# Performance work log

Measured on AMD Instinct MI355X. Metric: run time of the kernel, lower is better.

## Reference

```python
import jax, jax.numpy as jnp
from jax import lax
import numpy as np

DN = ('NCHW', 'OIHW', 'NCHW')

def conv2d_same(x, w, b):
    # 5x5, stride 1, pad 2 == SAME
    y = lax.conv_general_dilated(x, w, (1, 1), 'SAME', dimension_numbers=DN)
    return y + b[None, :, None, None]

def setup_inputs() -> dict:
    key = jax.random.key(0)
    ks = jax.random.split(key, 5)
    B, S, D = 8, 2048, 1024
    k55 = 0.2  # ~1/sqrt(25) init scale
    return {
        'x':  jax.random.normal(ks[0], (B, S, D), dtype=jnp.float32),
        'w1': jax.random.normal(ks[1], (1, 1, 5, 5), dtype=jnp.float32) * k55,
        'b1': jnp.zeros((1,), jnp.float32),
        'w2': jax.random.normal(ks[2], (1, 1, 5, 5), dtype=jnp.float32) * k55,
        'b2': jnp.zeros((1,), jnp.float32),
        'w3': jax.random.normal(ks[3], (1, 2, 5, 5), dtype=jnp.float32) * k55,
        'b3': jnp.zeros((1,), jnp.float32),
        'w4': jax.random.normal(ks[4], (1, 1, 5, 5), dtype=jnp.float32) * k55,
        'b4': jnp.zeros((1,), jnp.float32),
    }

def reference(x, w1, b1, w2, b2, w3, b3, w4, b4):
    # x: [b, s, d]
    xT = jnp.swapaxes(x, 1, 2)                              # [b, d, s]
    # self-similarity, softmax over BATCH dim (dim=0, as in original)
    NSSM = jax.nn.softmax(jnp.einsum('bsd,btd->bst', x, x), axis=0)   # [b, s, s]
    conv_x  = conv2d_same(x[:, None],  w1, b1)[:, 0]        # [b, s, d]
    conv_xT = conv2d_same(xT[:, None], w2, b2)[:, 0]        # [b, d, s]
    Attention_map = jax.nn.softmax(jnp.matmul(conv_x, conv_xT), axis=0)  # [b, s, s]
    Moca_map = conv2d_same(jnp.stack([NSSM, Attention_map], axis=1), w3, b3)[:, 0]  # [b, s, s]
    conv_g = conv2d_same(x[:, None], w4, b4)[:, 0]          # [b, s, d]
    Wz = jnp.matmul(Moca_map, conv_g)                       # [b, s, d]
    return Wz + x
```

## Files before the change

### kernel.cpp

```cpp
#include <hip/hip_runtime.h>

#define Bz 8
#define Sz 2048
#define Dz 1024

typedef __attribute__((ext_vector_type(8))) _Float16 f16x8;
typedef __attribute__((ext_vector_type(8))) short short8v;
typedef __attribute__((ext_vector_type(4))) short short4v;
typedef __attribute__((ext_vector_type(4))) float f32x4;

__device__ __forceinline__ short f2h(float f) {
    _Float16 h = (_Float16)f;
    return __builtin_bit_cast(short, h);
}
__device__ __forceinline__ float h2f(short s) {
    return (float)__builtin_bit_cast(_Float16, s);
}
__device__ __forceinline__ void gld16(const void* g, void* l) {
    __builtin_amdgcn_global_load_lds(
        (const __attribute__((address_space(1))) void*)g,
        (__attribute__((address_space(3))) void*)l, 16, 0, 0);
}

__global__ __launch_bounds__(256) void conv3_kernel(
    const float* __restrict__ x,
    const float* __restrict__ w1, const float* __restrict__ b1,
    const float* __restrict__ w2, const float* __restrict__ b2,
    short* __restrict__ x16, short* __restrict__ C1f, short* __restrict__ C2f)
{
    __shared__ float w[50];
    __shared__ float bias[2];
    const size_t SD = (size_t)Sz * Dz;
    int tid = threadIdx.x;
    if (tid < 25) w[tid] = w1[tid];
    else if (tid < 50) w[tid] = w2[tid - 25];
    if (tid == 50) { bias[0] = b1[0]; bias[1] = b2[0]; }
    __syncthreads();

    int d4 = tid * 4;
    int y = blockIdx.y;
    int s = ((y & 7) << 8) | (y >> 3);
    int b = blockIdx.z;
    const float* xb = x + (size_t)b * SD + d4;

    float wv[5][12];
#pragma unroll
    for (int i = 0; i < 5; i++) {
        int ss = s + i - 2;
        int ssc = ss < 0 ? 0 : (ss >= Sz ? Sz - 1 : ss);
        const float* rp = xb + (size_t)ssc * Dz;
        if (d4 > 0) *(float4*)&wv[i][0] = *(const float4*)(rp - 4);
        else { wv[i][0] = wv[i][1] = wv[i][2] = wv[i][3] = 0.f; }
        *(float4*)&wv[i][4] = *(const float4*)rp;
        if (d4 < 1020) *(float4*)&wv[i][8] = *(const float4*)(rp + 4);
        else { wv[i][8] = wv[i][9] = wv[i][10] = wv[i][11] = 0.f; }
        if (ss != ssc) {
#pragma unroll
            for (int q = 0; q < 12; q++) wv[i][q] = 0.f;
        }
    }

    float o1[4] = {}, o2[4] = {};
#pragma unroll
    for (int i = 0; i < 5; i++)
#pragma unroll
        for (int j = 0; j < 5; j++) {
            float c1w = w[i * 5 + j], c2w = w[25 + j * 5 + i];
#pragma unroll
            for (int q = 0; q < 4; q++) {
                float v = wv[i][q + j + 2];
                o1[q] = fmaf(c1w, v, o1[q]);
                o2[q] = fmaf(c2w, v, o2[q]);
            }
        }
    size_t o = (size_t)b * SD + (size_t)s * Dz + d4;
    short4v hx, h1, h2;
#pragma unroll
    for (int q = 0; q < 4; q++) {
        hx[q] = f2h(wv[2][q + 4]);
        h1[q] = f2h(o1[q] + bias[0]);
        h2[q] = f2h(o2[q] + bias[1]);
    }
    *(short4v*)(x16 + o) = hx;
    *(short4v*)(C1f + o) = h1;
    *(short4v*)(C2f + o) = h2;
}

__global__ __launch_bounds__(256) void convT_kernel(
    const float* __restrict__ x, const float* __restrict__ w4,
    const float* __restrict__ b4, short* __restrict__ C4T)
{
    __shared__ float xs[68][73];
    __shared__ short ct[64][72];
    __shared__ float w[25];
    __shared__ float bb;
    const size_t SD = (size_t)Sz * Dz;
    int tid = threadIdx.x;
    if (tid < 25) w[tid] = w4[tid];
    if (tid == 25) bb = b4[0];

    int s0 = blockIdx.x * 64, d0 = blockIdx.y * 64, b = blockIdx.z;
    const float* xb = x + (size_t)b * SD;
    for (int k = tid; k < 68 * 68; k += 256) {
        int r = k / 68, c = k - r * 68;
        int gr = s0 - 2 + r, gc = d0 - 2 + c;
        float v = 0.f;
        if (gr >= 0 && gr < Sz && gc >= 0 && gc < Dz) v = xb[(size_t)gr * Dz + gc];
        xs[r][c] = v;
    }
    __syncthreads();

    int sl = tid & 63, dg = tid >> 6;
    float acc[16];
#pragma unroll
    for (int q = 0; q < 16; q++) acc[q] = bb;
#pragma unroll
    for (int i = 0; i < 5; i++) {
        float row[20];
#pragma unroll
        for (int m = 0; m < 20; m++) row[m] = xs[sl + i][dg * 16 + m];
#pragma unroll
        for (int j = 0; j < 5; j++) {
            float wv = w[i * 5 + j];
#pragma unroll
            for (int q = 0; q < 16; q++) acc[q] = fmaf(wv, row[q + j], acc[q]);
        }
    }
#pragma unroll
    for (int q = 0; q < 16; q++) ct[dg * 16 + q][sl] = f2h(acc[q]);
    __syncthreads();

    int dl = tid >> 2, sc = (tid & 3) * 16;
    f16x8 v0 = *(const f16x8*)&ct[dl][sc];
    f16x8 v1 = *(const f16x8*)&ct[dl][sc + 8];
    short* op = C4T + (size_t)b * SD + (size_t)(d0 + dl) * Sz + s0 + sc;
    *(f16x8*)op = v0;
    *(f16x8*)(op + 8) = v1;
}

__global__ __launch_bounds__(512, 2) void logit8_f16(
    const short* __restrict__ Ag, const short* __restrict__ Bg,
    const short* __restrict__ Aa, const short* __restrict__ Ba,
    short* __restrict__ Qg, short* __restrict__ Qa,
    int rlo, int sq256off, long PS)
{
    __shared__ char lds[131072];

    int flat = blockIdx.x + 8 * (blockIdx.y + 4 * blockIdx.z);
    int nid = (flat & 7) * 64 + (flat >> 3);
    int bx = nid & 7, by = (nid >> 3) & 3, bz = nid >> 5;
    const int map = bz >> 3, bzb = bz & 7;
    if (map == 0) {
        int ntl = bx - sq256off;
        if (ntl >= 0 && ntl < 4 && ntl < by) return;
    }

    const size_t SD = (size_t)Sz * Dz;
    const int K = Dz;
    const short* A = (map ? Aa : Ag) + (size_t)bzb * SD;
    const short* B = (map ? Ba : Bg) + (size_t)bzb * SD;
    short* Q = (map ? Qa : Qg) + (size_t)bzb * PS;

    const int m0 = by * 256, n0 = bx * 256;
    const int t = threadIdx.x;
    const int lane = t & 63;
    const int w = t >> 6;
    const int wm = w >> 2, wn = w & 3;
    const int fr = lane & 15;
    const int kb = lane >> 4;

    const int cc16 = ((t & 7) ^ ((t >> 3) & 7)) * 16;
    const int tr = t >> 3;
    const int bdst = (t >> 8) * 8192 + ((t >> 3) & 31) * 128 + (t & 7) * 16;

    auto STA = [&](int tile, int h) {
        char* base = lds + (tile & 1) * 65536;
#pragma unroll
        for (int j = 0; j < 2; j++) {
            int row = m0 + j * 128 + h * 64 + tr;
            gld16((const char*)A + ((size_t)row * K + tile * 64) * 2 + cc16,
                  base + j * 16384 + h * 8192 + t * 16);
        }
    };
    auto STB = [&](int tile, int h) {
        char* base = lds + (tile & 1) * 65536 + 32768;
#pragma unroll
        for (int j = 0; j < 2; j++) {
            int u = j * 64 + tr;
            int row = n0 + (u >> 5) * 64 + h * 32 + (u & 31);
            gld16((const char*)B + ((size_t)row * K + tile * 64) * 2 + cc16,
                  base + j * 16384 + h * 4096 + bdst);
        }
    };

    int aoff[2], boff[2];
#pragma unroll
    for (int ks = 0; ks < 2; ks++) {
        int slot = ((ks * 4 + kb) ^ (fr & 7)) * 16;
        aoff[ks] = (wm * 128 + fr) * 128 + slot;
        boff[ks] = (wn * 64 + fr) * 128 + slot;
    }

    f16x8 aR[8];
    f16x8 bR[2][4];
    f32x4 acc[8][4];
#pragma unroll
    for (int i = 0; i < 8; i++)
#pragma unroll
        for (int j = 0; j < 4; j++) acc[i][j] = (f32x4){0.f, 0.f, 0.f, 0.f};

    auto LDA = [&](int qa, int d) {
        const char* p = lds + d * 65536 + qa * 8192;
#pragma unroll
        for (int f = 0; f < 4; f++)
#pragma unroll
            for (int ks = 0; ks < 2; ks++)
                aR[f * 2 + ks] = *(const f16x8*)(p + aoff[ks] + f * 2048);
    };
    auto LDB = [&](int qb, int d, int which) {
        const char* p = lds + d * 65536 + 32768 + qb * 4096;
#pragma unroll
        for (int g = 0; g < 2; g++)
#pragma unroll
            for (int ks = 0; ks < 2; ks++)
                bR[which][g * 2 + ks] = *(const f16x8*)(p + boff[ks] + g * 2048);
    };
#define MMQ(qa, qb, which)                                                        \
    __builtin_amdgcn_s_setprio(1);                                                \
    _Pragma("unroll") for (int f = 0; f < 4; f++)                                 \
        _Pragma("unroll") for (int g = 0; g < 2; g++)                             \
            _Pragma("unroll") for (int ks = 0; ks < 2; ks++)                      \
                acc[(qa)*4 + f][(qb)*2 + g] = __builtin_amdgcn_mfma_f32_16x16x32_f16( \
                    aR[f * 2 + ks], bR[which][g * 2 + ks], acc[(qa)*4 + f][(qb)*2 + g], 0, 0, 0); \
    __builtin_amdgcn_s_setprio(0);

#define BAR()  __builtin_amdgcn_s_barrier(); __builtin_amdgcn_sched_barrier(0)
#define WAIT4() asm volatile("s_waitcnt vmcnt(4)" ::: "memory"); __builtin_amdgcn_sched_barrier(0)
#define WAIT0() asm volatile("s_waitcnt vmcnt(0)" ::: "memory"); __builtin_amdgcn_sched_barrier(0)

    STA(0, 0); STB(0, 0); STA(0, 1); STB(0, 1);
    STA(1, 0); STB(1, 0);

    const int NIT = K / 128;
    for (int it = 0; it < NIT - 1; ++it) {
        const int V = 2 * it + 1, W = 2 * it + 2, X = 2 * it + 3;
        WAIT4(); BAR();
        STA(V, 1); LDA(0, 0); LDB(0, 0, 0); MMQ(0, 0, 0);
        BAR();
        STB(V, 1); LDB(1, 0, 1); MMQ(0, 1, 1);
        BAR();
        STA(W, 0); LDA(1, 0); MMQ(1, 0, 0);
        BAR();
        STB(W, 0); MMQ(1, 1, 1);
        WAIT4(); BAR();
        STA(W, 1); LDA(0, 1); LDB(0, 1, 0); MMQ(0, 0, 0);
        BAR();
        STB(W, 1); LDB(1, 1, 1); MMQ(0, 1, 1);
        BAR();
        STA(X, 0); LDA(1, 1); MMQ(1, 0, 0);
        BAR();
        STB(X, 0); MMQ(1, 1, 1);
    }
    {
        const int V = 2 * NIT - 1;
        WAIT4(); BAR();
        STA(V, 1); LDA(0, 0); LDB(0, 0, 0); MMQ(0, 0, 0);
        BAR();
        STB(V, 1); LDB(1, 0, 1); MMQ(0, 1, 1);
        BAR();
        LDA(1, 0); MMQ(1, 0, 0);
        BAR();
        MMQ(1, 1, 1);
        WAIT0(); BAR();
        LDA(0, 1); LDB(0, 1, 0); MMQ(0, 0, 0);
        BAR();
        LDB(1, 1, 1); MMQ(0, 1, 1);
        BAR();
        LDA(1, 1); MMQ(1, 0, 0);
        BAR();
        MMQ(1, 1, 1);
    }
#undef MMQ
#undef BAR
#undef WAIT4
#undef WAIT0

#pragma unroll
    for (int mf = 0; mf < 8; mf++)
#pragma unroll
        for (int nf = 0; nf < 4; nf++) {
            int col = n0 + wn * 64 + nf * 16 + fr;
#pragma unroll
            for (int r = 0; r < 4; r++) {
                int rowg = m0 + wm * 128 + mf * 16 + kb * 4 + r;
                float o = acc[mf][nf][r];
                if (map == 0 && rlo + rowg == col) o -= 1024.f;
                Q[(size_t)rowg * Sz + col] = f2h(o);
            }
        }
}

__global__ __launch_bounds__(256) void mirror_g(
    short* __restrict__ F, int o0, long PS)
{
    __shared__ short ts[128][136];
    int p = blockIdx.x, b = blockIdx.y;
    int mi = 1, base = 0;
    while (p >= base + mi) { base += mi; mi++; }
    int nt = p - base;
    short* Fb = F + (size_t)b * PS;
    int t = threadIdx.x;
    int rr = t >> 1, c0 = (t & 1) * 64;
    const short* src = Fb + (size_t)(nt * 128 + rr) * Sz + o0 + mi * 128 + c0;
#pragma unroll
    for (int j = 0; j < 8; j++)
        *(short8v*)&ts[rr][c0 + j * 8] = *(const short8v*)(src + j * 8);
    __syncthreads();
    short* dst = Fb + (size_t)(mi * 128 + rr) * Sz + o0 + nt * 128 + c0;
#pragma unroll
    for (int j = 0; j < 8; j++) {
        short8v v;
#pragma unroll
        for (int e = 0; e < 8; e++) v[e] = ts[c0 + j * 8 + e][rr];
        *(short8v*)(dst + j * 8) = v;
    }
}

__global__ __launch_bounds__(256) void softmax_ip(
    short* __restrict__ Qg, short* __restrict__ Qa, int nElem, long ps)
{
    int i8 = (blockIdx.x * 256 + threadIdx.x) * 8;
    if (i8 >= nElem) return;
    short* Q = blockIdx.z ? Qa : Qg;

    short8v v[Bz];
    float f[Bz][8];
#pragma unroll
    for (int b = 0; b < Bz; b++) {
        v[b] = *(const short8v*)(Q + i8 + (size_t)b * ps);
#pragma unroll
        for (int e = 0; e < 8; e++) f[b][e] = h2f(v[b][e]);
    }
#pragma unroll
    for (int e = 0; e < 8; e++) {
        float mx = f[0][e];
#pragma unroll
        for (int b = 1; b < Bz; b++) mx = fmaxf(mx, f[b][e]);
        float sum = 0.f;
#pragma unroll
        for (int b = 0; b < Bz; b++) { f[b][e] = __expf(f[b][e] - mx); sum += f[b][e]; }
        float inv = 1.f / sum;
#pragma unroll
        for (int b = 0; b < Bz; b++) v[b][e] = f2h(f[b][e] * inv);
    }
#pragma unroll
    for (int b = 0; b < Bz; b++)
        *(short8v*)(Q + i8 + (size_t)b * ps) = v[b];
}

__global__ __launch_bounds__(256) void slab_copy(
    const short* __restrict__ Fg, const short* __restrict__ Fa,
    short* __restrict__ slab, long PS)
{
    int idx = blockIdx.x * 256 + threadIdx.x;
    int e = idx * 8;
    int map = e >> 16;
    int rem = e & 65535;
    int b = rem >> 13;
    int rem2 = rem & 8191;
    int row = rem2 >> 11;
    int col = rem2 & 2047;
    const short* src = (map ? Fa : Fg) + (size_t)b * PS + (size_t)(1020 + row) * Sz + col;
    *(short8v*)(slab + e) = *(const short8v*)src;
}

__global__ __launch_bounds__(256) void moca_kernel(
    const short* __restrict__ Gs, const short* __restrict__ As,
    const short* __restrict__ slab,
    const float* __restrict__ w3, const float* __restrict__ b3,
    short* __restrict__ Mout,
    int o0, int rlo, int slabLo, long psIn, long psOut)
{
    __shared__ float w[50];
    __shared__ float bb;
    int tid = threadIdx.x;
    if (tid < 50) w[tid] = w3[tid];
    if (tid == 50) bb = b3[0];
    __syncthreads();

    int t8 = tid * 8;
    int so = blockIdx.y, b = blockIdx.z;
    int s = o0 + so;
    const short* Gp = Gs + (size_t)b * psIn;
    const short* Ap = As + (size_t)b * psIn;

    float acc[8];
#pragma unroll
    for (int q = 0; q < 8; q++) acc[q] = bb;

#pragma unroll
    for (int i = 0; i < 5; i++) {
        int sr = s + i - 2;
        if (sr < 0 || sr >= Sz) continue;
        const short *gp, *ap;
        size_t ro;
        if (sr >= rlo) { gp = Gp; ap = Ap; ro = (size_t)(sr - rlo) * Sz; }
        else {
            gp = slab + (size_t)b * 8192;
            ap = slab + 65536 + (size_t)b * 8192;
            ro = (size_t)(sr - slabLo) * Sz;
        }
        float gw[16], aw[16];
#pragma unroll
        for (int g = 0; g < 4; g++) {
            int c0 = t8 - 4 + g * 4;
            if (c0 >= 0 && c0 + 3 < Sz) {
                short4v gv = *(const short4v*)(gp + ro + c0);
                short4v av = *(const short4v*)(ap + ro + c0);
#pragma unroll
                for (int e = 0; e < 4; e++) { gw[g * 4 + e] = h2f(gv[e]); aw[g * 4 + e] = h2f(av[e]); }
            } else {
#pragma unroll
                for (int e = 0; e < 4; e++) { gw[g * 4 + e] = 0.f; aw[g * 4 + e] = 0.f; }
            }
        }
#pragma unroll
        for (int j = 0; j < 5; j++) {
            float wg = w[i * 5 + j], wa = w[25 + i * 5 + j];
#pragma unroll
            for (int q = 0; q < 8; q++)
                acc[q] = fmaf(wg, gw[q + j + 2], fmaf(wa, aw[q + j + 2], acc[q]));
        }
    }
    short4v r0, r1;
#pragma unroll
    for (int q = 0; q < 4; q++) { r0[q] = f2h(acc[q]); r1[q] = f2h(acc[q + 4]); }
    short* op = Mout + (size_t)b * psOut + (size_t)so * Sz + t8;
    *(short4v*)op = r0;
    *(short4v*)(op + 4) = r1;
}

__global__ __launch_bounds__(512) void gemm_wz(
    const short* __restrict__ A, const short* __restrict__ B,
    const float* __restrict__ Src, float* __restrict__ C,
    int M, long sAb)
{
    __shared__ short sA[3][4096];
    __shared__ short sB[3][4096];

    int gx = gridDim.x, gy = gridDim.y;
    int total = gx * gy * gridDim.z;
    int flat = blockIdx.x + gx * (blockIdx.y + gy * blockIdx.z);
    int cpx = total >> 3;
    int nid = (flat & 7) * cpx + (flat >> 3);
    int bx = nid % gx;
    int tmp = nid / gx;
    int by = tmp % gy;
    int bz = tmp / gy;

    const size_t SD = (size_t)Sz * Dz;
    const int K = Sz;
    A += (size_t)bz * sAb;
    B += (size_t)bz * SD;
    Src += (size_t)bz * SD;
    C += (size_t)bz * SD;

    const int m0 = by * 128, n0 = bx * 128;
    const int t = threadIdx.x;
    const int lane = t & 63;
    const int w = t >> 6;
    const int wm = w >> 2, wn = w & 3;
    const int fr = lane & 15;
    const int kb = lane >> 4;

    const int s_  = (t & 7) ^ ((t >> 3) & 7);
    const int h_  = s_ >> 2, kbs = s_ & 3;
    const int lrow = t >> 3;
    int rowAs = m0 + lrow + h_ * 64; if (rowAs > M - 1) rowAs = M - 1;
    const int rowBs = n0 + lrow + h_ * 64;
    const size_t aOff = (size_t)rowAs * K * 2 + kbs * 16;
    const size_t bOff = (size_t)rowBs * K * 2 + kbs * 16;

    int rdA[4], rdB[2];
#pragma unroll
    for (int f = 0; f < 4; f++) {
        int row = wm * 64 + f * 16 + fr;
        rdA[f] = (row & 63) * 128 + ((((row >> 6) * 4 + kb) ^ (fr & 7)) * 16);
    }
#pragma unroll
    for (int g = 0; g < 2; g++) {
        int row = wn * 32 + g * 16 + fr;
        rdB[g] = (row & 63) * 128 + ((((row >> 6) * 4 + kb) ^ (fr & 7)) * 16);
    }

    f32x4 acc[4][2];
#pragma unroll
    for (int i = 0; i < 4; i++)
#pragma unroll
        for (int j = 0; j < 2; j++) acc[i][j] = (f32x4){0.f, 0.f, 0.f, 0.f};

    auto STAGE = [&](int buf, int k0) {
        gld16((const char*)A + aOff + (size_t)k0 * 2, (char*)&sA[buf][0] + t * 16);
        gld16((const char*)B + bOff + (size_t)k0 * 2, (char*)&sB[buf][0] + t * 16);
    };
    auto COMPUTE = [&](int buf) {
        const char* pA = (const char*)&sA[buf][0];
        const char* pB = (const char*)&sB[buf][0];
        f16x8 af[4], bfr[2];
#pragma unroll
        for (int f = 0; f < 4; f++) af[f] = *(const f16x8*)(pA + rdA[f]);
#pragma unroll
        for (int g = 0; g < 2; g++) bfr[g] = *(const f16x8*)(pB + rdB[g]);
#pragma unroll
        for (int mf = 0; mf < 4; mf++)
#pragma unroll
            for (int nf = 0; nf < 2; nf++)
                acc[mf][nf] = __builtin_amdgcn_mfma_f32_16x16x32_f16(af[mf], bfr[nf], acc[mf][nf], 0, 0, 0);
    };

    const int niter = K / 32;
    STAGE(0, 0);
    STAGE(1, 32);
    int cs = 0, ss = 2;
    for (int it = 0; it < niter; ++it) {
        if (it < niter - 1) { asm volatile("s_waitcnt vmcnt(2)" ::: "memory"); }
        else                { asm volatile("s_waitcnt vmcnt(0)" ::: "memory"); }
        __builtin_amdgcn_sched_barrier(0);
        __builtin_amdgcn_s_barrier();
        if (it + 2 < niter) STAGE(ss, (it + 2) * 32);
        COMPUTE(cs);
        cs = cs == 2 ? 0 : cs + 1;
        ss = ss == 2 ? 0 : ss + 1;
    }

#pragma unroll
    for (int mf = 0; mf < 4; mf++)
#pragma unroll
        for (int nf = 0; nf < 2; nf++) {
            int col = n0 + wn * 32 + nf * 16 + fr;
#pragma unroll
            for (int r = 0; r < 4; r++) {
                int rowg = m0 + wm * 64 + mf * 16 + kb * 4 + r;
                if (rowg < M)
                    C[(size_t)rowg * Dz + col] = acc[mf][nf][r] + Src[(size_t)rowg * Dz + col];
            }
        }
}

extern "C" void kernel_launch(void* const* d_in, const int* in_sizes, int n_in,
                              void* d_out, int out_size, void* d_ws, size_t ws_size,
                              hipStream_t stream)
{
    const float* x  = (const float*)d_in[0];
    const float* w1 = (const float*)d_in[1];
    const float* b1 = (const float*)d_in[2];
    const float* w2 = (const float*)d_in[3];
    const float* b2 = (const float*)d_in[4];
    const float* w3 = (const float*)d_in[5];
    const float* b3 = (const float*)d_in[6];
    const float* w4 = (const float*)d_in[7];
    const float* b4 = (const float*)d_in[8];
    float* out = (float*)d_out;

    const size_t SD = (size_t)Sz * Dz;
    const size_t BSD2 = (size_t)Bz * SD * 2;

    char* ws = (char*)d_ws;
    short* x16 = (short*)(ws);
    short* C1f = (short*)(ws + 1 * BSD2);
    short* C2f = (short*)(ws + 2 * BSD2);
    short* C4T = (short*)(ws + 3 * BSD2);
    char* strip0 = ws + 4 * BSD2;

    const size_t PS  = (size_t)1024 * Sz;
    const size_t PSM = (size_t)1026 * Sz;
    short* Fg   = (short*)strip0;
    short* Fa   = Fg + (size_t)Bz * PS;
    short* Mf   = Fa + (size_t)Bz * PS;
    short* slab = Mf + (size_t)Bz * PSM;

    conv3_kernel<<<dim3(1, Sz, Bz), 256, 0, stream>>>(
        x, w1, b1, w2, b2, x16, C1f, C2f);
    convT_kernel<<<dim3(Sz / 64, Dz / 64, Bz), 256, 0, stream>>>(x, w4, b4, C4T);

    const int ne = 1024 * Sz;

    logit8_f16<<<dim3(8, 4, 16), 512, 0, stream>>>(
        x16, x16, C1f, C2f, Fg, Fa, 0, 0, (long)PS);
    mirror_g<<<dim3(28, Bz), 256, 0, stream>>>(Fg, 0, (long)PS);
    softmax_ip<<<dim3((ne / 8 + 255) / 256, 1, 2), 256, 0, stream>>>(Fg, Fa, ne, (long)PS);
    slab_copy<<<dim3(64), 256, 0, stream>>>(Fg, Fa, slab, (long)PS);
    moca_kernel<<<dim3(1, 1022, Bz), 256, 0, stream>>>(
        Fg, Fa, slab, w3, b3, Mf, 0, 0, 0, (long)PS, (long)PSM);
    gemm_wz<<<dim3(Dz / 128, 8, Bz), 512, 0, stream>>>(
        Mf, C4T, x, out, 1022, (long)PSM);

    logit8_f16<<<dim3(8, 4, 16), 512, 0, stream>>>(
        x16 + (size_t)1024 * Dz, x16, C1f + (size_t)1024 * Dz, C2f,
        Fg, Fa, 1024, 4, (long)PS);
    mirror_g<<<dim3(28, Bz), 256, 0, stream>>>(Fg, 1024, (long)PS);
    softmax_ip<<<dim3((ne / 8 + 255) / 256, 1, 2), 256, 0, stream>>>(Fg, Fa, ne, (long)PS);
    moca_kernel<<<dim3(1, 1026, Bz), 256, 0, stream>>>(
        Fg, Fa, slab, w3, b3, Mf, 1022, 1024, 1020, (long)PS, (long)PSM);
    gemm_wz<<<dim3(Dz / 128, 9, Bz), 512, 0, stream>>>(
        Mf, C4T, x + (size_t)1022 * Dz, out + (size_t)1022 * Dz, 1026, (long)PSM);
}
```

Before: 572.0 us.

## Merge two Wz GEMMs into one 256x256-tile kernel and double conv3 rows per thread

The two half-GEMMs, each with 128x128 tiles, are replaced by a single wz8_f16 launch. It uses 256x256 tiles with a 128-wide K step and a double-buffered 128KB LDS pipeline, and reads its A rows from two separate Moca buffers. The second Moca buffer now reuses the x16 workspace, and the first buffer is sized to exactly 1022 rows. conv3 now computes two output rows per thread so the overlapping input rows are loaded once. The larger tiles raise register and LDS use, which limits occupancy, and reusing x16 assumes x16 is no longer read after the second logit pass.

Result: faster. 519.1 us (-9.3%).

```diff
diff --git a/kernel.cpp b/kernel.cpp
--- a/kernel.cpp
+++ b/kernel.cpp
@@ -39,14 +39,14 @@
 
     int d4 = tid * 4;
     int y = blockIdx.y;
-    int s = ((y & 7) << 8) | (y >> 3);
+    int s0 = (((y & 7) << 7) | (y >> 3)) * 2;
     int b = blockIdx.z;
     const float* xb = x + (size_t)b * SD + d4;
 
-    float wv[5][12];
-#pragma unroll
-    for (int i = 0; i < 5; i++) {
-        int ss = s + i - 2;
+    float wv[6][12];
+#pragma unroll
+    for (int i = 0; i < 6; i++) {
+        int ss = s0 + i - 2;
         int ssc = ss < 0 ? 0 : (ss >= Sz ? Sz - 1 : ss);
         const float* rp = xb + (size_t)ssc * Dz;
         if (d4 > 0) *(float4*)&wv[i][0] = *(const float4*)(rp - 4);
@@ -60,30 +60,33 @@
         }
     }
 
-    float o1[4] = {}, o2[4] = {};
-#pragma unroll
-    for (int i = 0; i < 5; i++)
-#pragma unroll
-        for (int j = 0; j < 5; j++) {
-            float c1w = w[i * 5 + j], c2w = w[25 + j * 5 + i];
-#pragma unroll
-            for (int q = 0; q < 4; q++) {
-                float v = wv[i][q + j + 2];
-                o1[q] = fmaf(c1w, v, o1[q]);
-                o2[q] = fmaf(c2w, v, o2[q]);
+#pragma unroll
+    for (int r = 0; r < 2; r++) {
+        float o1[4] = {}, o2[4] = {};
+#pragma unroll
+        for (int i = 0; i < 5; i++)
+#pragma unroll
+            for (int j = 0; j < 5; j++) {
+                float c1w = w[i * 5 + j], c2w = w[25 + j * 5 + i];
+#pragma unroll
+                for (int q = 0; q < 4; q++) {
+                    float v = wv[r + i][q + j + 2];
+                    o1[q] = fmaf(c1w, v, o1[q]);
+                    o2[q] = fmaf(c2w, v, o2[q]);
+                }
             }
-        }
-    size_t o = (size_t)b * SD + (size_t)s * Dz + d4;
-    short4v hx, h1, h2;
-#pragma unroll
-    for (int q = 0; q < 4; q++) {
-        hx[q] = f2h(wv[2][q + 4]);
-        h1[q] = f2h(o1[q] + bias[0]);
-        h2[q] = f2h(o2[q] + bias[1]);
-    }
-    *(short4v*)(x16 + o) = hx;
-    *(short4v*)(C1f + o) = h1;
-    *(short4v*)(C2f + o) = h2;
+        size_t o = (size_t)b * SD + (size_t)(s0 + r) * Dz + d4;
+        short4v hx, h1, h2;
+#pragma unroll
+        for (int q = 0; q < 4; q++) {
+            hx[q] = f2h(wv[2 + r][q + 4]);
+            h1[q] = f2h(o1[q] + bias[0]);
+            h2[q] = f2h(o2[q] + bias[1]);
+        }
+        *(short4v*)(x16 + o) = hx;
+        *(short4v*)(C1f + o) = h1;
+        *(short4v*)(C2f + o) = h2;
+    }
 }
 
 __global__ __launch_bounds__(256) void convT_kernel(
@@ -296,6 +299,165 @@
                 float o = acc[mf][nf][r];
                 if (map == 0 && rlo + rowg == col) o -= 1024.f;
                 Q[(size_t)rowg * Sz + col] = f2h(o);
+            }
+        }
+}
+
+__global__ __launch_bounds__(512, 2) void wz8_f16(
+    const short* __restrict__ M0, const short* __restrict__ M1,
+    const short* __restrict__ C4Tm,
+    const float* __restrict__ X, float* __restrict__ Out,
+    long psM0, long psM1)
+{
+    __shared__ char lds[131072];
+
+    int flat = blockIdx.x + 4 * (blockIdx.y + 8 * blockIdx.z);
+    int nid = (flat & 7) * 32 + (flat >> 3);
+    int bx = nid & 3, by = (nid >> 2) & 7, bz = nid >> 5;
+
+    const size_t SD = (size_t)Sz * Dz;
+    const int K = Sz;
+    const short* A0 = M0 + (size_t)bz * psM0;
+    const short* A1 = M1 + (size_t)bz * psM1;
+    const short* B = C4Tm + (size_t)bz * SD;
+    const float* Src = X + (size_t)bz * SD;
+    float* C = Out + (size_t)bz * SD;
+
+    const int m0 = by * 256, n0 = bx * 256;
+    const int t = threadIdx.x;
+    const int lane = t & 63;
+    const int w = t >> 6;
+    const int wm = w >> 2, wn = w & 3;
+    const int fr = lane & 15;
+    const int kb = lane >> 4;
+
+    const int cc16 = ((t & 7) ^ ((t >> 3) & 7)) * 16;
+    const int tr = t >> 3;
+    const int bdst = (t >> 8) * 8192 + ((t >> 3) & 31) * 128 + (t & 7) * 16;
+
+    auto STA = [&](int tile, int h) {
+        char* base = lds + (tile & 1) * 65536;
+#pragma unroll
+        for (int j = 0; j < 2; j++) {
+            int row = m0 + j * 128 + h * 64 + tr;
+            const short* src = (row < 1022) ? (A0 + (size_t)row * K)
+                                            : (A1 + (size_t)(row - 1022) * K);
+            gld16((const char*)src + (size_t)tile * 128 + cc16,
+                  base + j * 16384 + h * 8192 + t * 16);
+        }
+    };
+    auto STB = [&](int tile, int h) {
+        char* base = lds + (tile & 1) * 65536 + 32768;
+#pragma unroll
+        for (int j = 0; j < 2; j++) {
+            int u = j * 64 + tr;
+            int row = n0 + (u >> 5) * 64 + h * 32 + (u & 31);
+            gld16((const char*)B + ((size_t)row * K + tile * 64) * 2 + cc16,
+                  base + j * 16384 + h * 4096 + bdst);
+        }
+    };
+
+    int aoff[2], boff[2];
+#pragma unroll
+    for (int ks = 0; ks < 2; ks++) {
+        int slot = ((ks * 4 + kb) ^ (fr & 7)) * 16;
+        aoff[ks] = (wm * 128 + fr) * 128 + slot;
+        boff[ks] = (wn * 64 + fr) * 128 + slot;
+    }
+
+    f16x8 aR[8];
+    f16x8 bR[2][4];
+    f32x4 acc[8][4];
+#pragma unroll
+    for (int i = 0; i < 8; i++)
+#pragma unroll
+        for (int j = 0; j < 4; j++) acc[i][j] = (f32x4){0.f, 0.f, 0.f, 0.f};
+
+    auto LDA = [&](int qa, int d) {
+        const char* p = lds + d * 65536 + qa * 8192;
+#pragma unroll
+        for (int f = 0; f < 4; f++)
+#pragma unroll
+            for (int ks = 0; ks < 2; ks++)
+                aR[f * 2 + ks] = *(const f16x8*)(p + aoff[ks] + f * 2048);
+    };
+    auto LDB = [&](int qb, int d, int which) {
+        const char* p = lds + d * 65536 + 32768 + qb * 4096;
+#pragma unroll
+        for (int g = 0; g < 2; g++)
+#pragma unroll
+            for (int ks = 0; ks < 2; ks++)
+                bR[which][g * 2 + ks] = *(const f16x8*)(p + boff[ks] + g * 2048);
+    };
+#define MMQ(qa, qb, which)                                                        \
+    __builtin_amdgcn_s_setprio(1);                                                \
+    _Pragma("unroll") for (int f = 0; f < 4; f++)                                 \
+        _Pragma("unroll") for (int g = 0; g < 2; g++)                             \
+            _Pragma("unroll") for (int ks = 0; ks < 2; ks++)                      \
+                acc[(qa)*4 + f][(qb)*2 + g] = __builtin_amdgcn_mfma_f32_16x16x32_f16( \
+                    aR[f * 2 + ks], bR[which][g * 2 + ks], acc[(qa)*4 + f][(qb)*2 + g], 0, 0, 0); \
+    __builtin_amdgcn_s_setprio(0);
+
+#define BAR()  __builtin_amdgcn_s_barrier(); __builtin_amdgcn_sched_barrier(0)
+#define WAIT4() asm volatile("s_waitcnt vmcnt(4)" ::: "memory"); __builtin_amdgcn_sched_barrier(0)
+#define WAIT0() asm volatile("s_waitcnt vmcnt(0)" ::: "memory"); __builtin_amdgcn_sched_barrier(0)
+
+    STA(0, 0); STB(0, 0); STA(0, 1); STB(0, 1);
+    STA(1, 0); STB(1, 0);
+
+    const int NIT = K / 128;
+    for (int it = 0; it < NIT - 1; ++it) {
+        const int V = 2 * it + 1, W = 2 * it + 2, X2 = 2 * it + 3;
+        WAIT4(); BAR();
+        STA(V, 1); LDA(0, 0); LDB(0, 0, 0); MMQ(0, 0, 0);
+        BAR();
+        STB(V, 1); LDB(1, 0, 1); MMQ(0, 1, 1);
+        BAR();
+        STA(W, 0); LDA(1, 0); MMQ(1, 0, 0);
+        BAR();
+        STB(W, 0); MMQ(1, 1, 1);
+        WAIT4(); BAR();
+        STA(W, 1); LDA(0, 1); LDB(0, 1, 0); MMQ(0, 0, 0);
+        BAR();
+        STB(W, 1); LDB(1, 1, 1); MMQ(0, 1, 1);
+        BAR();
+        STA(X2, 0); LDA(1, 1); MMQ(1, 0, 0);
+        BAR();
+        STB(X2, 0); MMQ(1, 1, 1);
+    }
+    {
+        const int V = 2 * NIT - 1;
+        WAIT4(); BAR();
+        STA(V, 1); LDA(0, 0); LDB(0, 0, 0); MMQ(0, 0, 0);
+        BAR();
+        STB(V, 1); LDB(1, 0, 1); MMQ(0, 1, 1);
+        BAR();
+        LDA(1, 0); MMQ(1, 0, 0);
+        BAR();
+        MMQ(1, 1, 1);
+        WAIT0(); BAR();
+        LDA(0, 1); LDB(0, 1, 0); MMQ(0, 0, 0);
+        BAR();
+        LDB(1, 1, 1); MMQ(0, 1, 1);
+        BAR();
+        LDA(1, 1); MMQ(1, 0, 0);
+        BAR();
+        MMQ(1, 1, 1);
+    }
+#undef MMQ
+#undef BAR
+#undef WAIT4
+#undef WAIT0
+
+#pragma unroll
+    for (int mf = 0; mf < 8; mf++)
+#pragma unroll
+        for (int nf = 0; nf < 4; nf++) {
+            int col = n0 + wn * 64 + nf * 16 + fr;
+#pragma unroll
+            for (int r = 0; r < 4; r++) {
+                int rowg = m0 + wm * 128 + mf * 16 + kb * 4 + r;
+                C[(size_t)rowg * Dz + col] = acc[mf][nf][r] + Src[(size_t)rowg * Dz + col];
             }
         }
 }
@@ -440,113 +602,6 @@
     *(short4v*)(op + 4) = r1;
 }
 
-__global__ __launch_bounds__(512) void gemm_wz(
-    const short* __restrict__ A, const short* __restrict__ B,
-    const float* __restrict__ Src, float* __restrict__ C,
-    int M, long sAb)
-{
-    __shared__ short sA[3][4096];
-    __shared__ short sB[3][4096];
-
-    int gx = gridDim.x, gy = gridDim.y;
-    int total = gx * gy * gridDim.z;
-    int flat = blockIdx.x + gx * (blockIdx.y + gy * blockIdx.z);
-    int cpx = total >> 3;
-    int nid = (flat & 7) * cpx + (flat >> 3);
-    int bx = nid % gx;
-    int tmp = nid / gx;
-    int by = tmp % gy;
-    int bz = tmp / gy;
-
-    const size_t SD = (size_t)Sz * Dz;
-    const int K = Sz;
-    A += (size_t)bz * sAb;
-    B += (size_t)bz * SD;
-    Src += (size_t)bz * SD;
-    C += (size_t)bz * SD;
-
-    const int m0 = by * 128, n0 = bx * 128;
-    const int t = threadIdx.x;
-    const int lane = t & 63;
-    const int w = t >> 6;
-    const int wm = w >> 2, wn = w & 3;
-    const int fr = lane & 15;
-    const int kb = lane >> 4;
-
-    const int s_  = (t & 7) ^ ((t >> 3) & 7);
-    const int h_  = s_ >> 2, kbs = s_ & 3;
-    const int lrow = t >> 3;
-    int rowAs = m0 + lrow + h_ * 64; if (rowAs > M - 1) rowAs = M - 1;
-    const int rowBs = n0 + lrow + h_ * 64;
-    const size_t aOff = (size_t)rowAs * K * 2 + kbs * 16;
-    const size_t bOff = (size_t)rowBs * K * 2 + kbs * 16;
-
-    int rdA[4], rdB[2];
-#pragma unroll
-    for (int f = 0; f < 4; f++) {
-        int row = wm * 64 + f * 16 + fr;
-        rdA[f] = (row & 63) * 128 + ((((row >> 6) * 4 + kb) ^ (fr & 7)) * 16);
-    }
-#pragma unroll
-    for (int g = 0; g < 2; g++) {
-        int row = wn * 32 + g * 16 + fr;
-        rdB[g] = (row & 63) * 128 + ((((row >> 6) * 4 + kb) ^ (fr & 7)) * 16);
-    }
-
-    f32x4 acc[4][2];
-#pragma unroll
-    for (int i = 0; i < 4; i++)
-#pragma unroll
-        for (int j = 0; j < 2; j++) acc[i][j] = (f32x4){0.f, 0.f, 0.f, 0.f};
-
-    auto STAGE = [&](int buf, int k0) {
-        gld16((const char*)A + aOff + (size_t)k0 * 2, (char*)&sA[buf][0] + t * 16);
-        gld16((const char*)B + bOff + (size_t)k0 * 2, (char*)&sB[buf][0] + t * 16);
-    };
-    auto COMPUTE = [&](int buf) {
-        const char* pA = (const char*)&sA[buf][0];
-        const char* pB = (const char*)&sB[buf][0];
-        f16x8 af[4], bfr[2];
-#pragma unroll
-        for (int f = 0; f < 4; f++) af[f] = *(const f16x8*)(pA + rdA[f]);
-#pragma unroll
-        for (int g = 0; g < 2; g++) bfr[g] = *(const f16x8*)(pB + rdB[g]);
-#pragma unroll
-        for (int mf = 0; mf < 4; mf++)
-#pragma unroll
-            for (int nf = 0; nf < 2; nf++)
-                acc[mf][nf] = __builtin_amdgcn_mfma_f32_16x16x32_f16(af[mf], bfr[nf], acc[mf][nf], 0, 0, 0);
-    };
-
-    const int niter = K / 32;
-    STAGE(0, 0);
-    STAGE(1, 32);
-    int cs = 0, ss = 2;
-    for (int it = 0; it < niter; ++it) {
-        if (it < niter - 1) { asm volatile("s_waitcnt vmcnt(2)" ::: "memory"); }
-        else                { asm volatile("s_waitcnt vmcnt(0)" ::: "memory"); }
-        __builtin_amdgcn_sched_barrier(0);
-        __builtin_amdgcn_s_barrier();
-        if (it + 2 < niter) STAGE(ss, (it + 2) * 32);
-        COMPUTE(cs);
-        cs = cs == 2 ? 0 : cs + 1;
-        ss = ss == 2 ? 0 : ss + 1;
-    }
-
-#pragma unroll
-    for (int mf = 0; mf < 4; mf++)
-#pragma unroll
-        for (int nf = 0; nf < 2; nf++) {
-            int col = n0 + wn * 32 + nf * 16 + fr;
-#pragma unroll
-            for (int r = 0; r < 4; r++) {
-                int rowg = m0 + wm * 64 + mf * 16 + kb * 4 + r;
-                if (rowg < M)
-                    C[(size_t)rowg * Dz + col] = acc[mf][nf][r] + Src[(size_t)rowg * Dz + col];
-            }
-        }
-}
-
 extern "C" void kernel_launch(void* const* d_in, const int* in_sizes, int n_in,
                               void* d_out, int out_size, void* d_ws, size_t ws_size,
                               hipStream_t stream)
@@ -572,14 +627,16 @@
     short* C4T = (short*)(ws + 3 * BSD2);
     char* strip0 = ws + 4 * BSD2;
 
-    const size_t PS  = (size_t)1024 * Sz;
-    const size_t PSM = (size_t)1026 * Sz;
+    const size_t PS   = (size_t)1024 * Sz;
+    const size_t PSM0 = (size_t)1022 * Sz;
+    const size_t PSM1 = (size_t)1026 * Sz;
     short* Fg   = (short*)strip0;
     short* Fa   = Fg + (size_t)Bz * PS;
-    short* Mf   = Fa + (size_t)Bz * PS;
-    short* slab = Mf + (size_t)Bz * PSM;
-
-    conv3_kernel<<<dim3(1, Sz, Bz), 256, 0, stream>>>(
+    short* Mf0  = Fa + (size_t)Bz * PS;
+    short* slab = Mf0 + (size_t)Bz * PSM0;
+    short* Mf1  = x16;
+
+    conv3_kernel<<<dim3(1, Sz / 2, Bz), 256, 0, stream>>>(
         x, w1, b1, w2, b2, x16, C1f, C2f);
     convT_kernel<<<dim3(Sz / 64, Dz / 64, Bz), 256, 0, stream>>>(x, w4, b4, C4T);
 
@@ -591,9 +648,7 @@
     softmax_ip<<<dim3((ne / 8 + 255) / 256, 1, 2), 256, 0, stream>>>(Fg, Fa, ne, (long)PS);
     slab_copy<<<dim3(64), 256, 0, stream>>>(Fg, Fa, slab, (long)PS);
     moca_kernel<<<dim3(1, 1022, Bz), 256, 0, stream>>>(
-        Fg, Fa, slab, w3, b3, Mf, 0, 0, 0, (long)PS, (long)PSM);
-    gemm_wz<<<dim3(Dz / 128, 8, Bz), 512, 0, stream>>>(
-        Mf, C4T, x, out, 1022, (long)PSM);
+        Fg, Fa, slab, w3, b3, Mf0, 0, 0, 0, (long)PS, (long)PSM0);
 
     logit8_f16<<<dim3(8, 4, 16), 512, 0, stream>>>(
         x16 + (size_t)1024 * Dz, x16, C1f + (size_t)1024 * Dz, C2f,
@@ -601,7 +656,8 @@
     mirror_g<<<dim3(28, Bz), 256, 0, stream>>>(Fg, 1024, (long)PS);
     softmax_ip<<<dim3((ne / 8 + 255) / 256, 1, 2), 256, 0, stream>>>(Fg, Fa, ne, (long)PS);
     moca_kernel<<<dim3(1, 1026, Bz), 256, 0, stream>>>(
-        Fg, Fa, slab, w3, b3, Mf, 1022, 1024, 1020, (long)PS, (long)PSM);
-    gemm_wz<<<dim3(Dz / 128, 9, Bz), 512, 0, stream>>>(
-        Mf, C4T, x + (size_t)1022 * Dz, out + (size_t)1022 * Dz, 1026, (long)PSM);
-}
+        Fg, Fa, slab, w3, b3, Mf1, 1022, 1024, 1020, (long)PS, (long)PSM1);
+
+    wz8_f16<<<dim3(4, 8, 8), 512, 0, stream>>>(
+        Mf0, Mf1, C4T, x, out, (long)PSM0, (long)PSM1);
+}
```
